# Optimization experiments

Measured on AMD Instinct MI355X. Metric: run time of the kernel, lower is better.

The kernel has to match this reference:

```python
import jax, jax.numpy as jnp
import numpy as np
from jax import lax

RADIUS = 3
ITERATION = 6
KSIZE = 2 * RADIUS + 1


def _make_kernels(r):
    # Build the 8 directional side-window box kernels, order: L,R,U,D,NW,NE,SW,SE
    k = 2 * r + 1
    f = np.ones((k, k), np.float32)
    L = f.copy(); L[:, r + 1:] = 0
    R = f.copy(); R[:, :r] = 0
    U = f.copy(); U[r + 1:, :] = 0
    D = f.copy(); D[:r, :] = 0
    NW = U.copy(); NW[:, r + 1:] = 0
    NE = U.copy(); NE[:, :r] = 0
    SW = D.copy(); SW[:, r + 1:] = 0
    SE = D.copy(); SE[:, :r] = 0
    n_half = (r + 1) * k          # normalizer for half windows
    n_quarter = (r + 1) ** 2      # normalizer for quarter windows
    ks = np.stack([L / n_half, R / n_half, U / n_half, D / n_half,
                   NW / n_quarter, NE / n_quarter, SW / n_quarter, SE / n_quarter])
    return jnp.asarray(ks[:, None, :, :])  # (8,1,k,k) OIHW


def setup_inputs() -> dict:
    key = jax.random.key(0)
    k1, k2 = jax.random.split(key)
    im = jax.random.normal(k1, (4, 3, 512, 512), dtype=jnp.float32)
    pert = jax.random.normal(k2, (4, 3, 512, 512), dtype=jnp.float32)
    return {"im": im, "pert": pert}


def reference(im, pert):
    b, c, h, w = im.shape
    W = _make_kernels(RADIUS)

    def conv8(x):  # (N,1,h,w) -> (N,8,h,w), SAME padding of radius
        return lax.conv_general_dilated(
            x, W, window_strides=(1, 1),
            padding=[(RADIUS, RADIUS), (RADIUS, RADIUS)],
            dimension_numbers=("NCHW", "OIHW", "NCHW"))

    # channels are processed independently with identical kernels -> fold c into batch
    im_f = im.reshape(b * c, 1, h, w)
    pert_f = pert.reshape(b * c, 1, h, w)

    def step(carry, _):
        im_ch, pert_ch = carry
        z = jnp.concatenate([im_ch, pert_ch], axis=0)  # (2N,1,h,w)
        dz = conv8(z) - z                              # (2N,8,h,w), broadcast over dir
        d, dd = jnp.split(dz, 2, axis=0)
        idx = jnp.argmin(jnp.abs(d), axis=1, keepdims=True)    # (N,1,h,w)
        dm = jnp.take_along_axis(d, idx, axis=1)
        ddm = jnp.take_along_axis(dd, idx, axis=1)
        return (im_ch + dm, pert_ch + ddm), None

    (im_f, pert_f), _ = lax.scan(step, (im_f, pert_f), None, length=ITERATION)
    # torch code overwrites every channel of res with pert_ch -> result is filtered pert
    return pert_f.reshape(b, c, h, w)
```

## Files before the change

### kernel.cpp

```cpp
#include <hip/hip_runtime.h>

#define HH 512
#define WW 512
#define NIMG 12
#define RAD 3
#define TW 64
#define TH 16
#define LW (TW + 2*RAD)
#define LH (TH + 2*RAD)

__global__ __launch_bounds__(256) void swf_step(
    const float* __restrict__ im_in, const float* __restrict__ pe_in,
    float* __restrict__ im_out, float* __restrict__ pe_out)
{
    __shared__ float sI[LH][LW];
    __shared__ float sP[LH][LW];
    __shared__ float hlP[LH][TW];
    __shared__ float hrP[LH][TW];

    const int tid = threadIdx.x;
    const int x0 = blockIdx.x * TW;
    const int y0 = blockIdx.y * TH;
    const size_t base = (size_t)blockIdx.z * (size_t)(HH * WW);
    const float* imb = im_in + base;
    const float* peb = pe_in + base;

    for (int i = tid; i < LH * LW; i += 256) {
        int r = i / LW;
        int c = i - r * LW;
        int gy = y0 - RAD + r;
        int gx = x0 - RAD + c;
        bool ok = ((unsigned)gy < (unsigned)HH) && ((unsigned)gx < (unsigned)WW);
        int gi = gy * WW + gx;
        sI[r][c] = ok ? imb[gi] : 0.0f;
        sP[r][c] = ok ? peb[gi] : 0.0f;
    }
    __syncthreads();

    for (int i = tid; i < LH * TW; i += 256) {
        int r = i >> 6;
        int c = i & 63;
        float b0 = sP[r][c],     b1 = sP[r][c + 1], b2 = sP[r][c + 2],
              b3 = sP[r][c + 3], b4 = sP[r][c + 4], b5 = sP[r][c + 5],
              b6 = sP[r][c + 6];
        hlP[r][c] = (b0 + b1) + (b2 + b3);
        hrP[r][c] = (b3 + b4) + (b5 + b6);
    }
    __syncthreads();

    const float w28 = 1.0f / 28.0f;
    const float w16 = 0.0625f;
    const int tx = tid & 63;
    const int ty = tid >> 6;

    for (int k = 0; k < 4; ++k) {
        const int oy = ty + 4 * k;

        float wi[7][7];
        #pragma unroll
        for (int dy = 0; dy < 7; ++dy)
            #pragma unroll
            for (int dx = 0; dx < 7; ++dx)
                wi[dy][dx] = sI[oy + dy][tx + dx];

        float d[8];
        {
            float sL = 0.f, sR = 0.f, sU = 0.f, sD = 0.f;
            float sNW = 0.f, sNE = 0.f, sSW = 0.f, sSE = 0.f;
            #pragma unroll
            for (int dy = 0; dy < 7; ++dy) {
                #pragma unroll
                for (int dx = 0; dx < 4; ++dx)
                    sL = fmaf(wi[dy][dx], w28, sL);
                #pragma unroll
                for (int dx = 3; dx < 7; ++dx)
                    sR = fmaf(wi[dy][dx], w28, sR);
            }
            #pragma unroll
            for (int dy = 0; dy < 4; ++dy) {
                #pragma unroll
                for (int dx = 0; dx < 7; ++dx)
                    sU = fmaf(wi[dy][dx], w28, sU);
                #pragma unroll
                for (int dx = 0; dx < 4; ++dx)
                    sNW = fmaf(wi[dy][dx], w16, sNW);
                #pragma unroll
                for (int dx = 3; dx < 7; ++dx)
                    sNE = fmaf(wi[dy][dx], w16, sNE);
            }
            #pragma unroll
            for (int dy = 3; dy < 7; ++dy) {
                #pragma unroll
                for (int dx = 0; dx < 7; ++dx)
                    sD = fmaf(wi[dy][dx], w28, sD);
                #pragma unroll
                for (int dx = 0; dx < 4; ++dx)
                    sSW = fmaf(wi[dy][dx], w16, sSW);
                #pragma unroll
                for (int dx = 3; dx < 7; ++dx)
                    sSE = fmaf(wi[dy][dx], w16, sSE);
            }
            const float cI = wi[3][3];
            d[0] = sL - cI;  d[1] = sR - cI;  d[2] = sU - cI;  d[3] = sD - cI;
            d[4] = sNW - cI; d[5] = sNE - cI; d[6] = sSW - cI; d[7] = sSE - cI;
        }

        float e[8];
        {
            float qnw = ((hlP[oy][tx] + hlP[oy + 1][tx]) + (hlP[oy + 2][tx] + hlP[oy + 3][tx]));
            float qsw = ((hlP[oy + 3][tx] + hlP[oy + 4][tx]) + (hlP[oy + 5][tx] + hlP[oy + 6][tx]));
            float qne = ((hrP[oy][tx] + hrP[oy + 1][tx]) + (hrP[oy + 2][tx] + hrP[oy + 3][tx]));
            float qse = ((hrP[oy + 3][tx] + hrP[oy + 4][tx]) + (hrP[oy + 5][tx] + hrP[oy + 6][tx]));
            float cu  = ((sP[oy][tx + 3] + sP[oy + 1][tx + 3]) + (sP[oy + 2][tx + 3] + sP[oy + 3][tx + 3]));
            float cd  = ((sP[oy + 3][tx + 3] + sP[oy + 4][tx + 3]) + (sP[oy + 5][tx + 3] + sP[oy + 6][tx + 3]));
            float hlc = hlP[oy + 3][tx];
            float hrc = hrP[oy + 3][tx];
            float cP  = sP[oy + 3][tx + 3];
            e[0] = (qnw + qsw - hlc) * w28 - cP;
            e[1] = (qne + qse - hrc) * w28 - cP;
            e[2] = (qnw + qne - cu)  * w28 - cP;
            e[3] = (qsw + qse - cd)  * w28 - cP;
            e[4] = qnw * w16 - cP;
            e[5] = qne * w16 - cP;
            e[6] = qsw * w16 - cP;
            e[7] = qse * w16 - cP;
        }

        float bestAbs = fabsf(d[0]);
        float bd = d[0];
        float be = e[0];
        #pragma unroll
        for (int j = 1; j < 8; ++j) {
            float a = fabsf(d[j]);
            bool take = a < bestAbs;
            bestAbs = take ? a : bestAbs;
            bd = take ? d[j] : bd;
            be = take ? e[j] : be;
        }

        const int gy = y0 + oy;
        const int gx = x0 + tx;
        const size_t gi = base + (size_t)gy * WW + gx;
        im_out[gi] = wi[3][3] + bd;
        pe_out[gi] = sP[oy + 3][tx + 3] + be;
    }
}

extern "C" void kernel_launch(void* const* d_in, const int* in_sizes, int n_in,
                              void* d_out, int out_size, void* d_ws, size_t ws_size,
                              hipStream_t stream) {
    const float* im0 = (const float*)d_in[0];
    const float* pe0 = (const float*)d_in[1];
    float* out = (float*)d_out;

    const size_t npix = (size_t)NIMG * HH * WW;
    float* imA = (float*)d_ws;
    float* imB = imA + npix;
    float* peA = imB + npix;
    float* peB = out;

    dim3 grid(WW / TW, HH / TH, NIMG);
    dim3 block(256);

    swf_step<<<grid, block, 0, stream>>>(im0, pe0, imA, peA);
    swf_step<<<grid, block, 0, stream>>>(imA, peA, imB, peB);
    swf_step<<<grid, block, 0, stream>>>(imB, peB, imA, peA);
    swf_step<<<grid, block, 0, stream>>>(imA, peA, imB, peB);
    swf_step<<<grid, block, 0, stream>>>(imB, peB, imA, peA);
    swf_step<<<grid, block, 0, stream>>>(imA, peA, imB, out);
}
```

Baseline: 241.2 us.

## Register-stream rows per wave with rolling window, drop shared horizontal-sum pass

Each wave now processes 8 consecutive output rows and keeps a rolling 7-row window of image values and the horizontal partial sums of pert in registers. Each new row is loaded from shared memory once instead of re-reading the full 7x7 window for every output row. The separate shared-memory pass for the horizontal sums, along with its barrier, is removed. Tile height doubles to 32 rows, which shrinks the halo overhead but halves the block count and raises register pressure.

```diff
diff --git a/kernel.cpp b/kernel.cpp
--- a/kernel.cpp
+++ b/kernel.cpp
@@ -5,9 +5,10 @@
 #define NIMG 12
 #define RAD 3
 #define TW 64
-#define TH 16
+#define TH 32
 #define LW (TW + 2*RAD)
 #define LH (TH + 2*RAD)
+#define RPW 8
 
 __global__ __launch_bounds__(256) void swf_step(
     const float* __restrict__ im_in, const float* __restrict__ pe_in,
@@ -15,8 +16,6 @@
 {
     __shared__ float sI[LH][LW];
     __shared__ float sP[LH][LW];
-    __shared__ float hlP[LH][TW];
-    __shared__ float hrP[LH][TW];
 
     const int tid = threadIdx.x;
     const int x0 = blockIdx.x * TW;
@@ -37,89 +36,92 @@
     }
     __syncthreads();
 
-    for (int i = tid; i < LH * TW; i += 256) {
-        int r = i >> 6;
-        int c = i & 63;
-        float b0 = sP[r][c],     b1 = sP[r][c + 1], b2 = sP[r][c + 2],
-              b3 = sP[r][c + 3], b4 = sP[r][c + 4], b5 = sP[r][c + 5],
-              b6 = sP[r][c + 6];
-        hlP[r][c] = (b0 + b1) + (b2 + b3);
-        hrP[r][c] = (b3 + b4) + (b5 + b6);
-    }
-    __syncthreads();
-
     const float w28 = 1.0f / 28.0f;
     const float w16 = 0.0625f;
     const int tx = tid & 63;
-    const int ty = tid >> 6;
+    const int wv = tid >> 6;
+    const int r0 = wv * RPW;
 
-    for (int k = 0; k < 4; ++k) {
-        const int oy = ty + 4 * k;
+    float wi[7][7];
+    float hl[7], hr[7], cc[7];
 
-        float wi[7][7];
+    #pragma unroll
+    for (int m = 0; m < 7; ++m) {
         #pragma unroll
-        for (int dy = 0; dy < 7; ++dy)
-            #pragma unroll
-            for (int dx = 0; dx < 7; ++dx)
-                wi[dy][dx] = sI[oy + dy][tx + dx];
+        for (int dx = 0; dx < 7; ++dx)
+            wi[m][dx] = sI[r0 + m][tx + dx];
+        float b0 = sP[r0 + m][tx],     b1 = sP[r0 + m][tx + 1],
+              b2 = sP[r0 + m][tx + 2], b3 = sP[r0 + m][tx + 3],
+              b4 = sP[r0 + m][tx + 4], b5 = sP[r0 + m][tx + 5],
+              b6 = sP[r0 + m][tx + 6];
+        hl[m] = (b0 + b1) + (b2 + b3);
+        hr[m] = (b3 + b4) + (b5 + b6);
+        cc[m] = b3;
+    }
 
+    #pragma unroll
+    for (int jj = 0; jj < RPW; ++jj) {
         float d[8];
         {
             float sL = 0.f, sR = 0.f, sU = 0.f, sD = 0.f;
             float sNW = 0.f, sNE = 0.f, sSW = 0.f, sSE = 0.f;
             #pragma unroll
             for (int dy = 0; dy < 7; ++dy) {
+                const int s = (jj + dy) % 7;
                 #pragma unroll
                 for (int dx = 0; dx < 4; ++dx)
-                    sL = fmaf(wi[dy][dx], w28, sL);
+                    sL = fmaf(wi[s][dx], w28, sL);
                 #pragma unroll
                 for (int dx = 3; dx < 7; ++dx)
-                    sR = fmaf(wi[dy][dx], w28, sR);
+                    sR = fmaf(wi[s][dx], w28, sR);
             }
             #pragma unroll
             for (int dy = 0; dy < 4; ++dy) {
+                const int s = (jj + dy) % 7;
                 #pragma unroll
                 for (int dx = 0; dx < 7; ++dx)
-                    sU = fmaf(wi[dy][dx], w28, sU);
+                    sU = fmaf(wi[s][dx], w28, sU);
                 #pragma unroll
                 for (int dx = 0; dx < 4; ++dx)
-                    sNW = fmaf(wi[dy][dx], w16, sNW);
+                    sNW = fmaf(wi[s][dx], w16, sNW);
                 #pragma unroll
                 for (int dx = 3; dx < 7; ++dx)
-                    sNE = fmaf(wi[dy][dx], w16, sNE);
+                    sNE = fmaf(wi[s][dx], w16, sNE);
             }
             #pragma unroll
             for (int dy = 3; dy < 7; ++dy) {
+                const int s = (jj + dy) % 7;
                 #pragma unroll
                 for (int dx = 0; dx < 7; ++dx)
-                    sD = fmaf(wi[dy][dx], w28, sD);
+                    sD = fmaf(wi[s][dx], w28, sD);
                 #pragma unroll
                 for (int dx = 0; dx < 4; ++dx)
-                    sSW = fmaf(wi[dy][dx], w16, sSW);
+                    sSW = fmaf(wi[s][dx], w16, sSW);
                 #pragma unroll
                 for (int dx = 3; dx < 7; ++dx)
-                    sSE = fmaf(wi[dy][dx], w16, sSE);
+                    sSE = fmaf(wi[s][dx], w16, sSE);
             }
-            const float cI = wi[3][3];
+            const float cI = wi[(jj + 3) % 7][3];
             d[0] = sL - cI;  d[1] = sR - cI;  d[2] = sU - cI;  d[3] = sD - cI;
             d[4] = sNW - cI; d[5] = sNE - cI; d[6] = sSW - cI; d[7] = sSE - cI;
         }
 
         float e[8];
+        const int p0 = (jj + 0) % 7, p1 = (jj + 1) % 7, p2 = (jj + 2) % 7,
+                  p3 = (jj + 3) % 7, p4 = (jj + 4) % 7, p5 = (jj + 5) % 7,
+                  p6 = (jj + 6) % 7;
         {
-            float qnw = ((hlP[oy][tx] + hlP[oy + 1][tx]) + (hlP[oy + 2][tx] + hlP[oy + 3][tx]));
-            float qsw = ((hlP[oy + 3][tx] + hlP[oy + 4][tx]) + (hlP[oy + 5][tx] + hlP[oy + 6][tx]));
-            float qne = ((hrP[oy][tx] + hrP[oy + 1][tx]) + (hrP[oy + 2][tx] + hrP[oy + 3][tx]));
-            float qse = ((hrP[oy + 3][tx] + hrP[oy + 4][tx]) + (hrP[oy + 5][tx] + hrP[oy + 6][tx]));
-            float cu  = ((sP[oy][tx + 3] + sP[oy + 1][tx + 3]) + (sP[oy + 2][tx + 3] + sP[oy + 3][tx + 3]));
-            float cd  = ((sP[oy + 3][tx + 3] + sP[oy + 4][tx + 3]) + (sP[oy + 5][tx + 3] + sP[oy + 6][tx + 3]));
-            float hlc = hlP[oy + 3][tx];
-            float hrc = hrP[oy + 3][tx];
-            float cP  = sP[oy + 3][tx + 3];
-            e[0] = (qnw + qsw - hlc) * w28 - cP;
-            e[1] = (qne + qse - hrc) * w28 - cP;
-            e[2] = (qnw + qne - cu)  * w28 - cP;
-            e[3] = (qsw + qse - cd)  * w28 - cP;
+            float qnw = ((hl[p0] + hl[p1]) + (hl[p2] + hl[p3]));
+            float qsw = ((hl[p3] + hl[p4]) + (hl[p5] + hl[p6]));
+            float qne = ((hr[p0] + hr[p1]) + (hr[p2] + hr[p3]));
+            float qse = ((hr[p3] + hr[p4]) + (hr[p5] + hr[p6]));
+            float cu  = ((cc[p0] + cc[p1]) + (cc[p2] + cc[p3]));
+            float cd  = ((cc[p3] + cc[p4]) + (cc[p5] + cc[p6]));
+            float cP  = cc[p3];
+            e[0] = (qnw + qsw - hl[p3]) * w28 - cP;
+            e[1] = (qne + qse - hr[p3]) * w28 - cP;
+            e[2] = (qnw + qne - cu)     * w28 - cP;
+            e[3] = (qsw + qse - cd)     * w28 - cP;
             e[4] = qnw * w16 - cP;
             e[5] = qne * w16 - cP;
             e[6] = qsw * w16 - cP;
@@ -138,11 +140,25 @@
             be = take ? e[j] : be;
         }
 
-        const int gy = y0 + oy;
+        const int gy = y0 + r0 + jj;
         const int gx = x0 + tx;
         const size_t gi = base + (size_t)gy * WW + gx;
-        im_out[gi] = wi[3][3] + bd;
-        pe_out[gi] = sP[oy + 3][tx + 3] + be;
+        im_out[gi] = wi[(jj + 3) % 7][3] + bd;
+        pe_out[gi] = cc[p3] + be;
+
+        if (jj < RPW - 1) {
+            const int m = r0 + jj + 7;
+            const int slot = jj % 7;
+            #pragma unroll
+            for (int dx = 0; dx < 7; ++dx)
+                wi[slot][dx] = sI[m][tx + dx];
+            float b0 = sP[m][tx],     b1 = sP[m][tx + 1], b2 = sP[m][tx + 2],
+                  b3 = sP[m][tx + 3], b4 = sP[m][tx + 4], b5 = sP[m][tx + 5],
+                  b6 = sP[m][tx + 6];
+            hl[slot] = (b0 + b1) + (b2 + b3);
+            hr[slot] = (b3 + b4) + (b5 + b6);
+            cc[slot] = b3;
+        }
     }
 }
 
```

After: 255.6 us. 5.9% more time.
